# Kernel tuning notes

Measured on AMD Instinct MI355X. Metric: run time of the kernel, lower is better.

## Reference

```python
import jax, jax.numpy as jnp
import numpy as np

NUM_HEADS = 16
DIM_K = 128
DIM_V = 128
ROPE_BASE = 10000.0


def rope(x):
    # x: [..., seq, d]; rotate-half convention
    d = x.shape[-1]
    seq = x.shape[-2]
    half = d // 2
    inv_freq = 1.0 / (ROPE_BASE ** (jnp.arange(0, half, dtype=jnp.float32) / half))
    ang = jnp.arange(seq, dtype=jnp.float32)[:, None] * inv_freq[None, :]  # [seq, half]
    cos, sin = jnp.cos(ang), jnp.sin(ang)
    x1, x2 = x[..., :half], x[..., half:]
    return jnp.concatenate([x1 * cos - x2 * sin, x1 * sin + x2 * cos], axis=-1)


def setup_inputs() -> dict:
    key = jax.random.key(0)
    ks = jax.random.split(key, 8)
    B, S, D = 2, 2048, 2048
    s = lambda fan_in: 1.0 / np.sqrt(fan_in)
    return {
        'q_in': jax.random.normal(ks[0], (B, S, D), jnp.float32),
        'k_in': jax.random.normal(ks[1], (B, S, D), jnp.float32),
        'v_in': jax.random.normal(ks[2], (B, S, D), jnp.float32),
        'mask': jnp.zeros((B, S), dtype=bool),
        'Wq': jax.random.normal(ks[3], (D, NUM_HEADS * DIM_K), jnp.float32) * s(D),
        'bq': jnp.zeros((NUM_HEADS * DIM_K,), jnp.float32),
        'Wk': jax.random.normal(ks[4], (D, DIM_K), jnp.float32) * s(D),
        'bk': jnp.zeros((DIM_K,), jnp.float32),
        'Wv': jax.random.normal(ks[5], (D, DIM_V), jnp.float32) * s(D),
        'bv': jnp.zeros((DIM_V,), jnp.float32),
        'Wo': jax.random.normal(ks[6], (NUM_HEADS * DIM_V, D), jnp.float32) * s(NUM_HEADS * DIM_V),
        'bo': jnp.zeros((D,), jnp.float32),
    }


def reference(q_in, k_in, v_in, mask, Wq, bq, Wk, bk, Wv, bv, Wo, bo):
    B, Sq, _ = q_in.shape
    Sk = k_in.shape[1]
    # projections: multi-head Q, single shared K/V head (MQA)
    q = (q_in @ Wq + bq).reshape(B, Sq, NUM_HEADS, DIM_K).transpose(0, 2, 1, 3)  # [B,H,Sq,dk]
    k = k_in @ Wk + bk  # [B,Sk,dk]
    v = v_in @ Wv + bv  # [B,Sk,dv]
    # inline RoPE on q and k
    q = rope(q)
    k = rope(k)
    scores = jnp.einsum('bhqd,bkd->bhqk', q, k) / np.sqrt(DIM_K)  # [B,H,Sq,Sk]
    # padding mask: True means masked out
    scores = jnp.where(mask[:, None, None, :], -jnp.inf, scores)
    # causal mask
    causal = jnp.triu(jnp.ones((Sq, Sk), dtype=bool), k=1)
    scores = jnp.where(causal[None, None], -jnp.inf, scores)
    weights = jax.nn.softmax(scores, axis=-1)
    attn = jnp.einsum('bhqk,bkd->bhqd', weights, v)  # [B,H,Sq,dv]
    attn = attn.transpose(0, 2, 1, 3).reshape(B, Sq, NUM_HEADS * DIM_V)
    return attn @ Wo + bo
```

## Files before the change

kernel.cpp:

```cpp
#include <hip/hip_runtime.h>

#define NHEADS 16
#define DKV 128
#define BB 2
#define SS 2048
#define DD 2048

typedef __attribute__((ext_vector_type(8))) short bf16x8;
typedef __attribute__((ext_vector_type(4))) short bf16x4;
typedef __attribute__((ext_vector_type(4))) float f32x4;
typedef __attribute__((ext_vector_type(8))) _Float16 f16x8;

#define QSCL 0.12752775f

__device__ __forceinline__ short f2bf(float x) {
  unsigned u = __builtin_bit_cast(unsigned, x);
  unsigned r = (u + 0x7fffu + ((u >> 16) & 1u)) >> 16;
  return (short)(unsigned short)r;
}
__device__ __forceinline__ float bf2f(short s) {
  unsigned u = ((unsigned)(unsigned short)s) << 16;
  return __builtin_bit_cast(float, u);
}
__device__ __forceinline__ unsigned pk2bf(float a, float b) {
#if __has_builtin(__builtin_amdgcn_cvt_pk_bf16_f32)
  typedef __attribute__((ext_vector_type(2))) __bf16 bf2_t;
  bf2_t r = __builtin_amdgcn_cvt_pk_bf16_f32(a, b);
  return __builtin_bit_cast(unsigned, r);
#else
  unsigned ua = __builtin_bit_cast(unsigned, a);
  unsigned ub = __builtin_bit_cast(unsigned, b);
  return ((ua + 0x8000u) >> 16) | ((ub + 0x8000u) & 0xffff0000u);
#endif
}
__device__ __forceinline__ unsigned pkf16(float a, float b) {
#if __has_builtin(__builtin_amdgcn_cvt_pkrtz)
  typedef __attribute__((ext_vector_type(2))) __fp16 h2_t;
  h2_t r = __builtin_amdgcn_cvt_pkrtz(a, b);
  return __builtin_bit_cast(unsigned, r);
#else
  _Float16 ha = (_Float16)a, hb = (_Float16)b;
  unsigned short ua = __builtin_bit_cast(unsigned short, ha);
  unsigned short ub = __builtin_bit_cast(unsigned short, hb);
  return (unsigned)ua | ((unsigned)ub << 16);
#endif
}
__device__ __forceinline__ float exp2fast(float x) {
#if __has_builtin(__builtin_amdgcn_exp2f)
  return __builtin_amdgcn_exp2f(x);
#else
  return exp2f(x);
#endif
}

__device__ __forceinline__ void async16(const void* g, void* l) {
  __builtin_amdgcn_global_load_lds(
      (__attribute__((address_space(1))) void*)g,
      (__attribute__((address_space(3))) void*)l, 16, 0, 0);
}

__global__ __launch_bounds__(256) void cvt_q(const float* __restrict__ x,
                                             short* __restrict__ y) {
  int idx = blockIdx.x * 256 + threadIdx.x;
  int g = idx * 8;
  float4 a = *(const float4*)(x + g);
  float4 b = *(const float4*)(x + g + 4);
  uint4 o = {pk2bf(a.x, a.y), pk2bf(a.z, a.w), pk2bf(b.x, b.y), pk2bf(b.z, b.w)};
  *(uint4*)(y + g) = o;
}

__global__ __launch_bounds__(256) void transpose_w2(
    const float* __restrict__ W0, short* __restrict__ Wt0,
    const float* __restrict__ W1, short* __restrict__ Wt1,
    int K, int N, float s0, float s1) {
  __shared__ float T[32][33];
  const float* W = blockIdx.z ? W1 : W0;
  short* Wt = blockIdx.z ? Wt1 : Wt0;
  const float scale = blockIdx.z ? s1 : s0;
  const int nt = blockIdx.x * 32;
  const int kt = blockIdx.y * 32;
  const int tx = threadIdx.x & 31;
  const int ty = threadIdx.x >> 5;
#pragma unroll
  for (int i = 0; i < 4; ++i)
    T[ty + i * 8][tx] = W[(size_t)(kt + ty + i * 8) * N + nt + tx];
  __syncthreads();
#pragma unroll
  for (int i = 0; i < 4; ++i)
    Wt[(size_t)(nt + ty + i * 8) * K + kt + tx] = f2bf(T[tx][ty + i * 8] * scale);
}

template <int AMODE>
__global__ __launch_bounds__(256) void gemm_as(
    const void* __restrict__ Ap, const short* __restrict__ Bt,
    const float* __restrict__ bias, void* __restrict__ Cp,
    int M, int N, int K, int KC, int cmode, float bscale) {
  __shared__ __align__(16) short As[128 * 32];
  __shared__ __align__(16) short Bs[128 * 32];
  const int tid = threadIdx.x;
  int bxi = blockIdx.x, byi = blockIdx.y;
  if (gridDim.x == 16 && gridDim.y == 32) {
    int L = byi * 16 + bxi;
    int i = L & 7, t = L >> 3;
    byi = 8 * (i >> 1) + (t & 7);
    bxi = 2 * (t >> 3) + (i & 1);
  }
  const int bm = byi * 128;
  const int bn = bxi * 128;
  const int kz = blockIdx.z;
  const int w = tid >> 6, lane = tid & 63;
  const int lm = lane & 15, q4 = lane >> 4;
  const int m0 = (w & 1) * 64, n0 = (w >> 1) * 64;

  f32x4 acc[4][4];
#pragma unroll
  for (int mi = 0; mi < 4; ++mi)
#pragma unroll
    for (int ni = 0; ni < 4; ++ni) acc[mi][ni] = (f32x4){0.f, 0.f, 0.f, 0.f};

  const int kbeg = kz * KC;
  const int kend = kbeg + KC;

  for (int k0 = kbeg; k0 < kend; k0 += 32) {
    __syncthreads();
    if (AMODE == 1) {
      const short* Ab = (const short*)Ap;
#pragma unroll
      for (int i = 0; i < 2; ++i) {
        int rA = (w * 2 + i) * 16 + (lane >> 2);
        int cA = (lane & 3) ^ (rA & 3);
        async16(Ab + (size_t)(bm + rA) * K + k0 + cA * 8, &As[(w * 2 + i) * 512]);
      }
    } else {
      const float* Af = (const float*)Ap;
      float4 av[4];
#pragma unroll
      for (int i = 0; i < 4; ++i) {
        int qd = tid + i * 256;
        int r = qd >> 3, cq = qd & 7;
        av[i] = *(const float4*)(Af + (size_t)(bm + r) * K + k0 + cq * 4);
      }
#pragma unroll
      for (int i = 0; i < 4; ++i) {
        int qd = tid + i * 256;
        int r = qd >> 3, cq = qd & 7;
        int ch = cq >> 1, hf = cq & 1;
        int pc = ch ^ (r & 3);
        bf16x4 t = {f2bf(av[i].x), f2bf(av[i].y), f2bf(av[i].z), f2bf(av[i].w)};
        *(bf16x4*)&As[r * 32 + pc * 8 + hf * 4] = t;
      }
    }
#pragma unroll
    for (int i = 0; i < 2; ++i) {
      int rB = (w * 2 + i) * 16 + (lane >> 2);
      int cB = (lane & 3) ^ (rB & 3);
      async16(Bt + (size_t)(bn + rB) * K + k0 + cB * 8, &Bs[(w * 2 + i) * 512]);
    }
    __syncthreads();

    bf16x8 af[4], bf[4];
#pragma unroll
    for (int mi = 0; mi < 4; ++mi)
      af[mi] = *(const bf16x8*)&As[(m0 + mi * 16 + lm) * 32 + ((q4 ^ (lm & 3)) * 8)];
#pragma unroll
    for (int ni = 0; ni < 4; ++ni)
      bf[ni] = *(const bf16x8*)&Bs[(n0 + ni * 16 + lm) * 32 + ((q4 ^ (lm & 3)) * 8)];
#pragma unroll
    for (int mi = 0; mi < 4; ++mi)
#pragma unroll
      for (int ni = 0; ni < 4; ++ni)
        acc[mi][ni] = __builtin_amdgcn_mfma_f32_16x16x32_bf16(
            af[mi], bf[ni], acc[mi][ni], 0, 0, 0);
  }

  if (cmode == 2) {
    float* Cf = (float*)Cp + (size_t)kz * M * N;
#pragma unroll
    for (int mi = 0; mi < 4; ++mi)
#pragma unroll
      for (int ni = 0; ni < 4; ++ni)
#pragma unroll
        for (int reg = 0; reg < 4; ++reg)
          Cf[(size_t)(bm + m0 + mi * 16 + q4 * 4 + reg) * N +
             (bn + n0 + ni * 16 + lm)] = acc[mi][ni][reg];
  } else {
#pragma unroll
    for (int mi = 0; mi < 4; ++mi)
#pragma unroll
      for (int ni = 0; ni < 4; ++ni)
#pragma unroll
        for (int reg = 0; reg < 4; ++reg) {
          int rowg = bm + m0 + mi * 16 + q4 * 4 + reg;
          int colg = bn + n0 + ni * 16 + lm;
          float val = acc[mi][ni][reg] + bias[colg] * bscale;
          if (cmode == 0)
            ((float*)Cp)[(size_t)rowg * N + colg] = val;
          else
            ((short*)Cp)[(size_t)rowg * N + colg] = f2bf(val);
        }
  }
}

#define SPLITK 4
__global__ __launch_bounds__(256) void gemm_kv(
    const float* __restrict__ Ak, const float* __restrict__ Av,
    const short* __restrict__ Btk, const short* __restrict__ Btv,
    float* __restrict__ kpart, float* __restrict__ vpart) {
  __shared__ __align__(16) short As[128 * 32];
  __shared__ __align__(16) short Bs[128 * 32];
  const int tid = threadIdx.x;
  const int bm = blockIdx.y * 128;
  const int z = blockIdx.z;
  const int kz = z & 3;
  const float* Af = (z >= 4) ? Av : Ak;
  const short* Bt = (z >= 4) ? Btv : Btk;
  float* Cf = ((z >= 4) ? vpart : kpart) + (size_t)kz * (4096 * 128);
  const int K = DD, N = DKV;
  const int w = tid >> 6, lane = tid & 63;
  const int lm = lane & 15, q4 = lane >> 4;
  const int m0 = (w & 1) * 64, n0 = (w >> 1) * 64;

  f32x4 acc[4][4];
#pragma unroll
  for (int mi = 0; mi < 4; ++mi)
#pragma unroll
    for (int ni = 0; ni < 4; ++ni) acc[mi][ni] = (f32x4){0.f, 0.f, 0.f, 0.f};

  const int kbeg = kz * (DD / SPLITK);
  const int kend = kbeg + DD / SPLITK;

  for (int k0 = kbeg; k0 < kend; k0 += 32) {
    __syncthreads();
    {
      float4 av[4];
#pragma unroll
      for (int i = 0; i < 4; ++i) {
        int qd = tid + i * 256;
        int r = qd >> 3, cq = qd & 7;
        av[i] = *(const float4*)(Af + (size_t)(bm + r) * K + k0 + cq * 4);
      }
#pragma unroll
      for (int i = 0; i < 4; ++i) {
        int qd = tid + i * 256;
        int r = qd >> 3, cq = qd & 7;
        int ch = cq >> 1, hf = cq & 1;
        int pc = ch ^ (r & 3);
        bf16x4 t = {f2bf(av[i].x), f2bf(av[i].y), f2bf(av[i].z), f2bf(av[i].w)};
        *(bf16x4*)&As[r * 32 + pc * 8 + hf * 4] = t;
      }
    }
#pragma unroll
    for (int i = 0; i < 2; ++i) {
      int rB = (w * 2 + i) * 16 + (lane >> 2);
      int cB = (lane & 3) ^ (rB & 3);
      async16(Bt + (size_t)rB * K + k0 + cB * 8, &Bs[(w * 2 + i) * 512]);
    }
    __syncthreads();

    bf16x8 af[4], bf[4];
#pragma unroll
    for (int mi = 0; mi < 4; ++mi)
      af[mi] = *(const bf16x8*)&As[(m0 + mi * 16 + lm) * 32 + ((q4 ^ (lm & 3)) * 8)];
#pragma unroll
    for (int ni = 0; ni < 4; ++ni)
      bf[ni] = *(const bf16x8*)&Bs[(n0 + ni * 16 + lm) * 32 + ((q4 ^ (lm & 3)) * 8)];
#pragma unroll
    for (int mi = 0; mi < 4; ++mi)
#pragma unroll
      for (int ni = 0; ni < 4; ++ni)
        acc[mi][ni] = __builtin_amdgcn_mfma_f32_16x16x32_bf16(
            af[mi], bf[ni], acc[mi][ni], 0, 0, 0);
  }

#pragma unroll
  for (int mi = 0; mi < 4; ++mi)
#pragma unroll
    for (int ni = 0; ni < 4; ++ni)
#pragma unroll
      for (int reg = 0; reg < 4; ++reg)
        Cf[(size_t)(bm + m0 + mi * 16 + q4 * 4 + reg) * N +
           (n0 + ni * 16 + lm)] = acc[mi][ni][reg];
}

__global__ __launch_bounds__(256) void kv_reduce(
    const float* __restrict__ kpart, const float* __restrict__ vpart,
    const float* __restrict__ bk, const float* __restrict__ bv,
    short* __restrict__ kp, short* __restrict__ vtb,
    const unsigned char* __restrict__ m, float* __restrict__ mb) {
  __shared__ float Kt[32][128];
  __shared__ short Vl[128][36];
  const int tid = threadIdx.x;
  const int r0 = blockIdx.x * 32;
  if (tid < 32) mb[r0 + tid] = m[r0 + tid] ? -1e30f : 0.0f;
#pragma unroll
  for (int i = 0; i < 16; ++i) {
    int e = tid + i * 256;
    int r = e >> 7, c = e & 127;
    float sk = 0.f, sv = 0.f;
#pragma unroll
    for (int z = 0; z < SPLITK; ++z) {
      sk += kpart[((size_t)z * 4096 + r0 + r) * 128 + c];
      sv += vpart[((size_t)z * 4096 + r0 + r) * 128 + c];
    }
    Kt[r][c] = sk + bk[c];
    Vl[c][r] = f2bf(sv + bv[c]);
  }
  __syncthreads();
#pragma unroll
  for (int i = 0; i < 8; ++i) {
    int e = tid + i * 256;
    int r = e >> 6, d = e & 63;
    float x1 = Kt[r][d], x2 = Kt[r][d + 64];
    float s = (float)((r0 + r) & (SS - 1));
    float ang = s * exp2fast((float)d * (-13.287712379549449f / 64.0f));
    float sn, cs;
    __sincosf(ang, &sn, &cs);
    kp[(size_t)(r0 + r) * 128 + d] = f2bf(x1 * cs - x2 * sn);
    kp[(size_t)(r0 + r) * 128 + d + 64] = f2bf(x1 * sn + x2 * cs);
  }
  const int b = r0 >> 11;
  const int j = tid >> 1, soff = (tid & 1) * 16;
  short* dst = vtb + ((size_t)b * 128 + j) * SS + (r0 & (SS - 1)) + soff;
#pragma unroll
  for (int t = 0; t < 2; ++t) {
    bf16x8 tmp;
#pragma unroll
    for (int u = 0; u < 8; ++u) tmp[u] = Vl[j][soff + t * 8 + u];
    *(bf16x8*)(dst + t * 8) = tmp;
  }
}

#define PSTR 40

__global__ __launch_bounds__(512, 4) void flash_kernel(
    const short* __restrict__ q, const short* __restrict__ k,
    const short* __restrict__ vt, const float* __restrict__ mb,
    short* __restrict__ out, short* __restrict__ pO, float* __restrict__ pL) {
  __shared__ __align__(16) short Kb[2][32 * 128];
  __shared__ __align__(16) short Vb[2][128 * 64];
  __shared__ __align__(16) short Ps[8][16 * PSTR];
  const int j = blockIdx.x;
  const int cls = j >> 5, hb = j & 31;
  int qx, c;
  if (cls < 8) {
    qx = cls + 8; c = 0;
  } else {
    int kk = (cls - 8) >> 1;
    if ((cls & 1) == 0) { qx = 15 - kk; c = 1; }
    else                { qx = 7 - kk;  c = 0; }
  }
  const int h = hb & 15, b = hb >> 4;
  const int kt0 = c ? 32 : 0;
  int kend = 4 * qx + 4;
  if (c == 0 && kend > 32) kend = 32;

  const int tid = threadIdx.x;
  const int w = tid >> 6, lane = tid & 63;
  const int lm = lane & 15, q4 = lane >> 4;
  const int qrow0 = qx * 128 + w * 16;

  bf16x8 qf[4];
#pragma unroll
  for (int ks = 0; ks < 4; ++ks)
    qf[ks] = *(const bf16x8*)(q +
        ((size_t)b * SS + qrow0 + lm) * (NHEADS * DKV) + h * DKV +
        ks * 32 + q4 * 8);
  {
    float s = (float)(qrow0 + lm);
#pragma unroll
    for (int ks = 0; ks < 2; ++ks) {
      bf16x8 x1 = qf[ks], x2 = qf[ks + 2];
      bf16x8 y1, y2;
#pragma unroll
      for (int jj = 0; jj < 8; ++jj) {
        int d = ks * 32 + q4 * 8 + jj;
        float ang = s * exp2fast((float)d * (-13.287712379549449f / 64.0f));
        float sn, cs;
        __sincosf(ang, &sn, &cs);
        float a = bf2f(x1[jj]), b2 = bf2f(x2[jj]);
        y1[jj] = f2bf(a * cs - b2 * sn);
        y2[jj] = f2bf(a * sn + b2 * cs);
      }
      qf[ks] = y1;
      qf[ks + 2] = y2;
    }
  }

  bf16x8 onesb;
#pragma unroll
  for (int jj = 0; jj < 8; ++jj) onesb[jj] = (short)0x3F80;

  f32x4 O[8], Ol;
#pragma unroll
  for (int vi = 0; vi < 8; ++vi) O[vi] = (f32x4){0.f, 0.f, 0.f, 0.f};
  Ol = (f32x4){0.f, 0.f, 0.f, 0.f};

  const size_t kbase = (size_t)b * SS;

  {
    {
      int r = w * 4 + (lane >> 4);
      int cc = (lane & 15) ^ (r & 7);
      async16(k + (kbase + (size_t)kt0 * 32 + r) * DKV + cc * 8,
              &Kb[0][w * 512]);
    }
#pragma unroll
    for (int i = 0; i < 2; ++i) {
      int rV = (w * 2 + i) * 8 + (lane >> 3);
      int cV = (lane & 7) ^ (rV & 7);
      async16(vt + ((size_t)b * DKV + rV) * SS + (size_t)kt0 * 32 + cV * 8,
              &Vb[0][(w * 2 + i) * 512]);
    }
  }
  f32x4 mc0 = *(const f32x4*)(mb + kbase + (size_t)kt0 * 32 + q4 * 4);
  f32x4 mc1 = *(const f32x4*)(mb + kbase + (size_t)kt0 * 32 + 16 + q4 * 4);

  for (int kt = kt0; kt < kend; ++kt) {
    __syncthreads();

    f32x4 mn0, mn1;
    if (kt + 1 < kend) {
      const int t = kt + 1;
      {
        int r = w * 4 + (lane >> 4);
        int cc = (lane & 15) ^ (r & 7);
        async16(k + (kbase + (size_t)t * 32 + r) * DKV + cc * 8,
                &Kb[t & 1][w * 512]);
      }
      if (kt & 1) {
#pragma unroll
        for (int i = 0; i < 2; ++i) {
          int rV = (w * 2 + i) * 8 + (lane >> 3);
          int cV = (lane & 7) ^ (rV & 7);
          async16(vt + ((size_t)b * DKV + rV) * SS + (size_t)t * 32 + cV * 8,
                  &Vb[(t >> 1) & 1][(w * 2 + i) * 512]);
        }
      }
      mn0 = *(const f32x4*)(mb + kbase + (size_t)t * 32 + q4 * 4);
      mn1 = *(const f32x4*)(mb + kbase + (size_t)t * 32 + 16 + q4 * 4);
    }

    const short* Kc = Kb[kt & 1];
    f32x4 sacc[2];
#pragma unroll
    for (int mi = 0; mi < 2; ++mi) sacc[mi] = (f32x4){0.f, 0.f, 0.f, 0.f};
#pragma unroll
    for (int mi = 0; mi < 2; ++mi)
#pragma unroll
      for (int ks = 0; ks < 4; ++ks) {
        bf16x8 kf = *(const bf16x8*)&Kc[(mi * 16 + lm) * 128 +
                                        (((ks * 4 + q4) ^ (lm & 7)) << 3)];
        sacc[mi] = __builtin_amdgcn_mfma_f32_16x16x32_bf16(
            kf, qf[ks], sacc[mi], 0, 0, 0);
      }

    const bool diag = (kt >= 4 * qx);
#pragma unroll
    for (int mi = 0; mi < 2; ++mi) {
      f32x4 mbv = mi ? mc1 : mc0;
      float pv[4];
#pragma unroll
      for (int reg = 0; reg < 4; ++reg) {
        float s = sacc[mi][reg] + mbv[reg];
        if (diag) {
          int kg = kt * 32 + mi * 16 + q4 * 4 + reg;
          int qg = qrow0 + lm;
          if (kg > qg) s = -1e30f;
        }
        pv[reg] = exp2fast(s);
      }
      uint2 pkd = {pk2bf(pv[0], pv[1]), pk2bf(pv[2], pv[3])};
      *(uint2*)&Ps[w][lm * PSTR + mi * 16 + q4 * 4] = pkd;
    }
    mc0 = mn0;
    mc1 = mn1;

    const short* Vc = Vb[(kt >> 1) & 1];
    const int hf4 = (kt & 1) * 4;
    bf16x8 pf = *(const bf16x8*)&Ps[w][lm * PSTR + q4 * 8];
    Ol = __builtin_amdgcn_mfma_f32_16x16x32_bf16(pf, onesb, Ol, 0, 0, 0);
#pragma unroll
    for (int vi = 0; vi < 8; ++vi) {
      bf16x8 vf = *(const bf16x8*)&Vc[(vi * 16 + lm) * 64 +
                                      (((hf4 + q4) ^ (lm & 7)) << 3)];
      O[vi] = __builtin_amdgcn_mfma_f32_16x16x32_bf16(pf, vf, O[vi], 0, 0, 0);
    }
  }

  __syncthreads();
  float* Wr = (float*)&Vb[0][0] + w * 544;
  float linv[4];
#pragma unroll
  for (int reg = 0; reg < 4; ++reg) linv[reg] = 1.0f / Ol[reg];

  const bool split = (qx >= 8);
  short* obase;
  int ostr;
  if (split) {
    int slot = ((b * 16 + h) * 8 + (qx - 8)) * 2 + c;
    obase = pO + (size_t)slot * (128 * 128);
    ostr = 128;
    if (lm == 0) {
      float* dl = pL + (size_t)slot * 128 + w * 16;
#pragma unroll
      for (int reg = 0; reg < 4; ++reg)
        dl[q4 * 4 + reg] = Ol[reg];
    }
  } else {
    obase = out + ((size_t)b * SS + qx * 128) * (NHEADS * DKV) + h * DKV;
    ostr = NHEADS * DKV;
  }

#pragma unroll
  for (int qd = 0; qd < 4; ++qd) {
#pragma unroll
    for (int v2 = 0; v2 < 2; ++v2) {
      int vi = qd * 2 + v2;
#pragma unroll
      for (int reg = 0; reg < 4; ++reg)
        Wr[(q4 * 4 + reg) * 34 + v2 * 16 + lm] = O[vi][reg] * linv[reg];
    }
    int r = lane & 15, hh = lane >> 4;
    f32x4 t0 = *(const f32x4*)&Wr[r * 34 + hh * 8];
    f32x4 t1 = *(const f32x4*)&Wr[r * 34 + hh * 8 + 4];
    size_t oaddr = (size_t)(w * 16 + r) * ostr + qd * 32 + hh * 8;
    uint4 o0;
    if (split) {
      o0 = (uint4){pkf16(t0[0], t0[1]), pkf16(t0[2], t0[3]),
                   pkf16(t1[0], t1[1]), pkf16(t1[2], t1[3])};
    } else {
      o0 = (uint4){pk2bf(t0[0], t0[1]), pk2bf(t0[2], t0[3]),
                   pk2bf(t1[0], t1[1]), pk2bf(t1[2], t1[3])};
    }
    *(uint4*)(obase + oaddr) = o0;
  }
}

__global__ __launch_bounds__(256) void combine(
    const short* __restrict__ pO, const float* __restrict__ pL,
    short* __restrict__ out) {
  const int qxi = blockIdx.x, h = blockIdx.y, b = blockIdx.z;
  const int qx = 8 + qxi;
  const int slot2 = ((b * 16 + h) * 8 + qxi) * 2;
  const _Float16* p0 = (const _Float16*)(pO + (size_t)slot2 * (128 * 128));
  const _Float16* p1 = p0 + 128 * 128;
  const float* l0 = pL + (size_t)slot2 * 128;
  const float* l1 = l0 + 128;
  const int t = threadIdx.x;
  const int row = t >> 1, half = t & 1;
  const float w0 = l0[row], w1 = l1[row];
  const float inv = 1.0f / (w0 + w1);
  const float a0 = w0 * inv, a1 = w1 * inv;
  const int off = row * 128 + half * 64;
  short* dst = out + ((size_t)(b * SS + qx * 128 + row)) * (NHEADS * DKV) +
               h * DKV + half * 64;
#pragma unroll
  for (int v = 0; v < 8; ++v) {
    f16x8 x0 = *(const f16x8*)(p0 + off + v * 8);
    f16x8 x1 = *(const f16x8*)(p1 + off + v * 8);
    float r[8];
#pragma unroll
    for (int u = 0; u < 8; ++u)
      r[u] = (float)x0[u] * a0 + (float)x1[u] * a1;
    uint4 o = {pk2bf(r[0], r[1]), pk2bf(r[2], r[3]),
               pk2bf(r[4], r[5]), pk2bf(r[6], r[7])};
    *(uint4*)(dst + v * 8) = o;
  }
}

extern "C" void kernel_launch(void* const* d_in, const int* in_sizes, int n_in,
                              void* d_out, int out_size, void* d_ws, size_t ws_size,
                              hipStream_t stream) {
  const float* q_in = (const float*)d_in[0];
  const float* k_in = (const float*)d_in[1];
  const float* v_in = (const float*)d_in[2];
  const unsigned char* mask = (const unsigned char*)d_in[3];
  const float* Wq = (const float*)d_in[4];
  const float* bq = (const float*)d_in[5];
  const float* Wk = (const float*)d_in[6];
  const float* bk = (const float*)d_in[7];
  const float* Wv = (const float*)d_in[8];
  const float* bv = (const float*)d_in[9];
  const float* Wo = (const float*)d_in[10];
  const float* bo = (const float*)d_in[11];

  const int M = BB * SS;
  short* Wqt = (short*)d_ws;
  short* Wot = Wqt + (size_t)DD * DD;
  short* Wkt = Wot + (size_t)DD * DD;
  short* Wvt = Wkt + (size_t)DKV * DD;
  short* qb  = Wvt + (size_t)DKV * DD;
  short* qp  = qb + (size_t)M * DD;
  short* kp  = qp + (size_t)M * DD;
  short* vtb = kp + (size_t)M * DKV;
  float* mb  = (float*)(vtb + (size_t)BB * DKV * SS);
  float* kpart = mb + (size_t)BB * SS;
  float* vpart = kpart + (size_t)SPLITK * M * DKV;
  float* pL = vpart + (size_t)SPLITK * M * DKV;
  short* ap = qb;
  short* pO = (short*)kpart;

  cvt_q<<<M * DD / (8 * 256), 256, 0, stream>>>(q_in, qb);
  transpose_w2<<<dim3(DD / 32, DD / 32, 2), 256, 0, stream>>>(
      Wq, Wqt, Wo, Wot, DD, DD, QSCL, 1.0f);
  transpose_w2<<<dim3(DKV / 32, DD / 32, 2), 256, 0, stream>>>(
      Wk, Wkt, Wv, Wvt, DD, DKV, 1.0f, 1.0f);

  gemm_kv<<<dim3(1, M / 128, 2 * SPLITK), 256, 0, stream>>>(
      k_in, v_in, Wkt, Wvt, kpart, vpart);
  gemm_as<1><<<dim3(DD / 128, M / 128, 1), 256, 0, stream>>>(
      qb, Wqt, bq, qp, M, DD, DD, DD, 1, QSCL);
  kv_reduce<<<M / 32, 256, 0, stream>>>(kpart, vpart, bk, bv, kp, vtb, mask, mb);

  flash_kernel<<<dim3(768), 512, 0, stream>>>(qp, kp, vtb, mb, ap, pO, pL);
  combine<<<dim3(8, NHEADS, BB), 256, 0, stream>>>(pO, pL, ap);

  gemm_as<1><<<dim3(DD / 128, M / 128, 1), 256, 0, stream>>>(
      ap, Wot, bo, d_out, M, DD, DD, DD, 0, 1.0f);
}
```

Before: 387.7 us.

## Merge prep kernels and fuse K/V split-K GEMM with Q projection launch

Combines the q conversion and the two weight-transpose launches into one prep kernel that selects its work by block id. The split-K K/V GEMM and the Q projection GEMM are merged into one 768-block launch, with a grouped tile mapping for the Q part. kv_reduce is halved to 16 rows per block so it launches twice as many blocks. The aim is to cut launch overhead and the tail idle time between small kernels. The cost is a more divergent kernel and the risk of load imbalance between the different block types.

```diff
diff --git a/kernel.cpp b/kernel.cpp
--- a/kernel.cpp
+++ b/kernel.cpp
@@ -59,26 +59,50 @@
       (__attribute__((address_space(3))) void*)l, 16, 0, 0);
 }
 
-__global__ __launch_bounds__(256) void cvt_q(const float* __restrict__ x,
-                                             short* __restrict__ y) {
-  int idx = blockIdx.x * 256 + threadIdx.x;
-  int g = idx * 8;
-  float4 a = *(const float4*)(x + g);
-  float4 b = *(const float4*)(x + g + 4);
-  uint4 o = {pk2bf(a.x, a.y), pk2bf(a.z, a.w), pk2bf(b.x, b.y), pk2bf(b.z, b.w)};
-  *(uint4*)(y + g) = o;
-}
-
-__global__ __launch_bounds__(256) void transpose_w2(
-    const float* __restrict__ W0, short* __restrict__ Wt0,
-    const float* __restrict__ W1, short* __restrict__ Wt1,
-    int K, int N, float s0, float s1) {
+__global__ __launch_bounds__(256) void prep(
+    const float* __restrict__ q_in, short* __restrict__ qb,
+    const float* __restrict__ Wq, short* __restrict__ Wqt,
+    const float* __restrict__ Wo, short* __restrict__ Wot,
+    const float* __restrict__ Wk, short* __restrict__ Wkt,
+    const float* __restrict__ Wv, short* __restrict__ Wvt) {
+  const int id = blockIdx.x;
+  if (id < 4096) {
+    int idx = id * 256 + threadIdx.x;
+    int g = idx * 8;
+    float4 a = *(const float4*)(q_in + g);
+    float4 b = *(const float4*)(q_in + g + 4);
+    uint4 o = {pk2bf(a.x, a.y), pk2bf(a.z, a.w), pk2bf(b.x, b.y),
+               pk2bf(b.z, b.w)};
+    *(uint4*)(qb + g) = o;
+    return;
+  }
   __shared__ float T[32][33];
-  const float* W = blockIdx.z ? W1 : W0;
-  short* Wt = blockIdx.z ? Wt1 : Wt0;
-  const float scale = blockIdx.z ? s1 : s0;
-  const int nt = blockIdx.x * 32;
-  const int kt = blockIdx.y * 32;
+  const float* W;
+  short* Wt;
+  float scale = 1.0f;
+  int N, bx, by;
+  if (id < 12288) {
+    int Lt = id - 4096;
+    int z = Lt >> 12;
+    int rem = Lt & 4095;
+    bx = rem & 63;
+    by = rem >> 6;
+    N = DD;
+    if (z == 0) { W = Wq; Wt = Wqt; scale = QSCL; }
+    else        { W = Wo; Wt = Wot; }
+  } else {
+    int Ls = id - 12288;
+    int z = Ls >> 8;
+    int rem = Ls & 255;
+    bx = rem & 3;
+    by = rem >> 2;
+    N = DKV;
+    if (z == 0) { W = Wk; Wt = Wkt; }
+    else        { W = Wv; Wt = Wvt; }
+  }
+  const int K = DD;
+  const int nt = bx * 32;
+  const int kt = by * 32;
   const int tx = threadIdx.x & 31;
   const int ty = threadIdx.x >> 5;
 #pragma unroll
@@ -202,23 +226,19 @@
 }
 
 #define SPLITK 4
-__global__ __launch_bounds__(256) void gemm_kv(
-    const float* __restrict__ Ak, const float* __restrict__ Av,
+__global__ __launch_bounds__(256) void gemm_qkv(
+    const float* __restrict__ k_in, const float* __restrict__ v_in,
     const short* __restrict__ Btk, const short* __restrict__ Btv,
-    float* __restrict__ kpart, float* __restrict__ vpart) {
+    float* __restrict__ kpart, float* __restrict__ vpart,
+    const short* __restrict__ qb, const short* __restrict__ Wqt,
+    const float* __restrict__ bq, short* __restrict__ qp) {
   __shared__ __align__(16) short As[128 * 32];
   __shared__ __align__(16) short Bs[128 * 32];
   const int tid = threadIdx.x;
-  const int bm = blockIdx.y * 128;
-  const int z = blockIdx.z;
-  const int kz = z & 3;
-  const float* Af = (z >= 4) ? Av : Ak;
-  const short* Bt = (z >= 4) ? Btv : Btk;
-  float* Cf = ((z >= 4) ? vpart : kpart) + (size_t)kz * (4096 * 128);
-  const int K = DD, N = DKV;
   const int w = tid >> 6, lane = tid & 63;
   const int lm = lane & 15, q4 = lane >> 4;
   const int m0 = (w & 1) * 64, n0 = (w >> 1) * 64;
+  const int id = blockIdx.x;
 
   f32x4 acc[4][4];
 #pragma unroll
@@ -226,60 +246,120 @@
 #pragma unroll
     for (int ni = 0; ni < 4; ++ni) acc[mi][ni] = (f32x4){0.f, 0.f, 0.f, 0.f};
 
-  const int kbeg = kz * (DD / SPLITK);
-  const int kend = kbeg + DD / SPLITK;
-
-  for (int k0 = kbeg; k0 < kend; k0 += 32) {
-    __syncthreads();
-    {
-      float4 av[4];
-#pragma unroll
-      for (int i = 0; i < 4; ++i) {
-        int qd = tid + i * 256;
-        int r = qd >> 3, cq = qd & 7;
-        av[i] = *(const float4*)(Af + (size_t)(bm + r) * K + k0 + cq * 4);
-      }
-#pragma unroll
-      for (int i = 0; i < 4; ++i) {
-        int qd = tid + i * 256;
-        int r = qd >> 3, cq = qd & 7;
-        int ch = cq >> 1, hf = cq & 1;
-        int pc = ch ^ (r & 3);
-        bf16x4 t = {f2bf(av[i].x), f2bf(av[i].y), f2bf(av[i].z), f2bf(av[i].w)};
-        *(bf16x4*)&As[r * 32 + pc * 8 + hf * 4] = t;
-      }
-    }
-#pragma unroll
-    for (int i = 0; i < 2; ++i) {
-      int rB = (w * 2 + i) * 16 + (lane >> 2);
-      int cB = (lane & 3) ^ (rB & 3);
-      async16(Bt + (size_t)rB * K + k0 + cB * 8, &Bs[(w * 2 + i) * 512]);
-    }
-    __syncthreads();
-
-    bf16x8 af[4], bf[4];
+  if (id < 256) {
+    const int ym = id & 31, zz = id >> 5;
+    const int kz = zz & 3;
+    const float* Af = (zz >= 4) ? v_in : k_in;
+    const short* Bt = (zz >= 4) ? Btv : Btk;
+    float* Cf = ((zz >= 4) ? vpart : kpart) + (size_t)kz * (4096 * 128);
+    const int bm = ym * 128;
+    const int K = DD, N = DKV;
+    const int kbeg = kz * (DD / SPLITK);
+    const int kend = kbeg + DD / SPLITK;
+
+    for (int k0 = kbeg; k0 < kend; k0 += 32) {
+      __syncthreads();
+      {
+        float4 av[4];
+#pragma unroll
+        for (int i = 0; i < 4; ++i) {
+          int qd = tid + i * 256;
+          int r = qd >> 3, cq = qd & 7;
+          av[i] = *(const float4*)(Af + (size_t)(bm + r) * K + k0 + cq * 4);
+        }
+#pragma unroll
+        for (int i = 0; i < 4; ++i) {
+          int qd = tid + i * 256;
+          int r = qd >> 3, cq = qd & 7;
+          int ch = cq >> 1, hf = cq & 1;
+          int pc = ch ^ (r & 3);
+          bf16x4 t = {f2bf(av[i].x), f2bf(av[i].y), f2bf(av[i].z), f2bf(av[i].w)};
+          *(bf16x4*)&As[r * 32 + pc * 8 + hf * 4] = t;
+        }
+      }
+#pragma unroll
+      for (int i = 0; i < 2; ++i) {
+        int rB = (w * 2 + i) * 16 + (lane >> 2);
+        int cB = (lane & 3) ^ (rB & 3);
+        async16(Bt + (size_t)rB * K + k0 + cB * 8, &Bs[(w * 2 + i) * 512]);
+      }
+      __syncthreads();
+
+      bf16x8 af[4], bf[4];
+#pragma unroll
+      for (int mi = 0; mi < 4; ++mi)
+        af[mi] = *(const bf16x8*)&As[(m0 + mi * 16 + lm) * 32 + ((q4 ^ (lm & 3)) * 8)];
+#pragma unroll
+      for (int ni = 0; ni < 4; ++ni)
+        bf[ni] = *(const bf16x8*)&Bs[(n0 + ni * 16 + lm) * 32 + ((q4 ^ (lm & 3)) * 8)];
+#pragma unroll
+      for (int mi = 0; mi < 4; ++mi)
+#pragma unroll
+        for (int ni = 0; ni < 4; ++ni)
+          acc[mi][ni] = __builtin_amdgcn_mfma_f32_16x16x32_bf16(
+              af[mi], bf[ni], acc[mi][ni], 0, 0, 0);
+    }
+
 #pragma unroll
     for (int mi = 0; mi < 4; ++mi)
-      af[mi] = *(const bf16x8*)&As[(m0 + mi * 16 + lm) * 32 + ((q4 ^ (lm & 3)) * 8)];
-#pragma unroll
-    for (int ni = 0; ni < 4; ++ni)
-      bf[ni] = *(const bf16x8*)&Bs[(n0 + ni * 16 + lm) * 32 + ((q4 ^ (lm & 3)) * 8)];
+#pragma unroll
+      for (int ni = 0; ni < 4; ++ni)
+#pragma unroll
+        for (int reg = 0; reg < 4; ++reg)
+          Cf[(size_t)(bm + m0 + mi * 16 + q4 * 4 + reg) * N +
+             (n0 + ni * 16 + lm)] = acc[mi][ni][reg];
+  } else {
+    int L = id - 256;
+    int i2 = L & 7, t2 = L >> 3;
+    const int byi = 8 * (i2 >> 1) + (t2 & 7);
+    const int bxi = 2 * (t2 >> 3) + (i2 & 1);
+    const int bm = byi * 128;
+    const int bn = bxi * 128;
+    const int K = DD, N = DD;
+
+    for (int k0 = 0; k0 < DD; k0 += 32) {
+      __syncthreads();
+#pragma unroll
+      for (int i = 0; i < 2; ++i) {
+        int rA = (w * 2 + i) * 16 + (lane >> 2);
+        int cA = (lane & 3) ^ (rA & 3);
+        async16(qb + (size_t)(bm + rA) * K + k0 + cA * 8, &As[(w * 2 + i) * 512]);
+      }
+#pragma unroll
+      for (int i = 0; i < 2; ++i) {
+        int rB = (w * 2 + i) * 16 + (lane >> 2);
+        int cB = (lane & 3) ^ (rB & 3);
+        async16(Wqt + (size_t)(bn + rB) * K + k0 + cB * 8, &Bs[(w * 2 + i) * 512]);
+      }
+      __syncthreads();
+
+      bf16x8 af[4], bf[4];
+#pragma unroll
+      for (int mi = 0; mi < 4; ++mi)
+        af[mi] = *(const bf16x8*)&As[(m0 + mi * 16 + lm) * 32 + ((q4 ^ (lm & 3)) * 8)];
+#pragma unroll
+      for (int ni = 0; ni < 4; ++ni)
+        bf[ni] = *(const bf16x8*)&Bs[(n0 + ni * 16 + lm) * 32 + ((q4 ^ (lm & 3)) * 8)];
+#pragma unroll
+      for (int mi = 0; mi < 4; ++mi)
+#pragma unroll
+        for (int ni = 0; ni < 4; ++ni)
+          acc[mi][ni] = __builtin_amdgcn_mfma_f32_16x16x32_bf16(
+              af[mi], bf[ni], acc[mi][ni], 0, 0, 0);
+    }
+
 #pragma unroll
     for (int mi = 0; mi < 4; ++mi)
 #pragma unroll
       for (int ni = 0; ni < 4; ++ni)
-        acc[mi][ni] = __builtin_amdgcn_mfma_f32_16x16x32_bf16(
-            af[mi], bf[ni], acc[mi][ni], 0, 0, 0);
-  }
-
-#pragma unroll
-  for (int mi = 0; mi < 4; ++mi)
-#pragma unroll
-    for (int ni = 0; ni < 4; ++ni)
-#pragma unroll
-      for (int reg = 0; reg < 4; ++reg)
-        Cf[(size_t)(bm + m0 + mi * 16 + q4 * 4 + reg) * N +
-           (n0 + ni * 16 + lm)] = acc[mi][ni][reg];
+#pragma unroll
+        for (int reg = 0; reg < 4; ++reg) {
+          int rowg = bm + m0 + mi * 16 + q4 * 4 + reg;
+          int colg = bn + n0 + ni * 16 + lm;
+          qp[(size_t)rowg * N + colg] =
+              f2bf(acc[mi][ni][reg] + bq[colg] * QSCL);
+        }
+  }
 }
 
 __global__ __launch_bounds__(256) void kv_reduce(
@@ -287,13 +367,13 @@
     const float* __restrict__ bk, const float* __restrict__ bv,
     short* __restrict__ kp, short* __restrict__ vtb,
     const unsigned char* __restrict__ m, float* __restrict__ mb) {
-  __shared__ float Kt[32][128];
-  __shared__ short Vl[128][36];
+  __shared__ float Kt[16][128];
+  __shared__ short Vl[128][18];
   const int tid = threadIdx.x;
-  const int r0 = blockIdx.x * 32;
-  if (tid < 32) mb[r0 + tid] = m[r0 + tid] ? -1e30f : 0.0f;
-#pragma unroll
-  for (int i = 0; i < 16; ++i) {
+  const int r0 = blockIdx.x * 16;
+  if (tid < 16) mb[r0 + tid] = m[r0 + tid] ? -1e30f : 0.0f;
+#pragma unroll
+  for (int i = 0; i < 8; ++i) {
     int e = tid + i * 256;
     int r = e >> 7, c = e & 127;
     float sk = 0.f, sv = 0.f;
@@ -307,7 +387,7 @@
   }
   __syncthreads();
 #pragma unroll
-  for (int i = 0; i < 8; ++i) {
+  for (int i = 0; i < 4; ++i) {
     int e = tid + i * 256;
     int r = e >> 6, d = e & 63;
     float x1 = Kt[r][d], x2 = Kt[r][d + 64];
@@ -319,15 +399,12 @@
     kp[(size_t)(r0 + r) * 128 + d + 64] = f2bf(x1 * sn + x2 * cs);
   }
   const int b = r0 >> 11;
-  const int j = tid >> 1, soff = (tid & 1) * 16;
+  const int j = tid >> 1, soff = (tid & 1) * 8;
   short* dst = vtb + ((size_t)b * 128 + j) * SS + (r0 & (SS - 1)) + soff;
-#pragma unroll
-  for (int t = 0; t < 2; ++t) {
-    bf16x8 tmp;
-#pragma unroll
-    for (int u = 0; u < 8; ++u) tmp[u] = Vl[j][soff + t * 8 + u];
-    *(bf16x8*)(dst + t * 8) = tmp;
-  }
+  bf16x8 tmp;
+#pragma unroll
+  for (int u = 0; u < 8; ++u) tmp[u] = Vl[j][soff + u];
+  *(bf16x8*)dst = tmp;
 }
 
 #define PSTR 40
@@ -600,17 +677,11 @@
   short* ap = qb;
   short* pO = (short*)kpart;
 
-  cvt_q<<<M * DD / (8 * 256), 256, 0, stream>>>(q_in, qb);
-  transpose_w2<<<dim3(DD / 32, DD / 32, 2), 256, 0, stream>>>(
-      Wq, Wqt, Wo, Wot, DD, DD, QSCL, 1.0f);
-  transpose_w2<<<dim3(DKV / 32, DD / 32, 2), 256, 0, stream>>>(
-      Wk, Wkt, Wv, Wvt, DD, DKV, 1.0f, 1.0f);
-
-  gemm_kv<<<dim3(1, M / 128, 2 * SPLITK), 256, 0, stream>>>(
-      k_in, v_in, Wkt, Wvt, kpart, vpart);
-  gemm_as<1><<<dim3(DD / 128, M / 128, 1), 256, 0, stream>>>(
-      qb, Wqt, bq, qp, M, DD, DD, DD, 1, QSCL);
-  kv_reduce<<<M / 32, 256, 0, stream>>>(kpart, vpart, bk, bv, kp, vtb, mask, mb);
+  prep<<<12800, 256, 0, stream>>>(q_in, qb, Wq, Wqt, Wo, Wot, Wk, Wkt, Wv, Wvt);
+
+  gemm_qkv<<<768, 256, 0, stream>>>(k_in, v_in, Wkt, Wvt, kpart, vpart,
+                                    qb, Wqt, bq, qp);
+  kv_reduce<<<M / 16, 256, 0, stream>>>(kpart, vpart, bk, bv, kp, vtb, mask, mb);
 
   flash_kernel<<<dim3(768), 512, 0, stream>>>(qp, kp, vtb, mb, ap, pO, pL);
   combine<<<dim3(8, NHEADS, BB), 256, 0, stream>>>(pO, pL, ap);
```

Measured after the change: 363.4 us. 6.3% less time.
